# Performance work log

Measured on AMD Instinct MI355X. Metric: run time of the kernel, lower is better.

Reference implementation:

```python
import jax, jax.numpy as jnp
import numpy as np

N_EMBD = 512
N_HEAD = 8
D_HEAD = N_EMBD // N_HEAD
N_EXPERTS = 4
TOP_K = 2
D_FF = 4 * N_EMBD
EPS_RMS = 1e-5


def setup_inputs() -> dict:
    key = jax.random.key(0)
    ks = jax.random.split(key, 10)
    B, T, C = 8, 1024, N_EMBD
    s = 0.02
    return {
        "x": jax.random.normal(ks[0], (B, T, C), jnp.float32),
        "ln1_w": jnp.ones((C,), jnp.float32),
        "ln2_w": jnp.ones((C,), jnp.float32),
        "wq": jax.random.normal(ks[1], (C, C), jnp.float32) * s,
        "wk": jax.random.normal(ks[2], (C, C), jnp.float32) * s,
        "wv": jax.random.normal(ks[3], (C, C), jnp.float32) * s,
        "wo": jax.random.normal(ks[4], (C, C), jnp.float32) * s,
        "gate_w": jax.random.normal(ks[5], (N_EXPERTS, C), jnp.float32) * s,
        "w_fc": jax.random.normal(ks[6], (N_EXPERTS, D_FF, C), jnp.float32) * s,
        "w_proj": jax.random.normal(ks[7], (N_EXPERTS, C, D_FF), jnp.float32) * s,
    }


def rms_norm(x, w):
    var = jnp.mean(x * x, axis=-1, keepdims=True)
    return x * jax.lax.rsqrt(var + EPS_RMS) * w


def causal_attention(x, wq, wk, wv, wo):
    B, T, C = x.shape
    q = (x @ wq.T).reshape(B, T, N_HEAD, D_HEAD)
    k = (x @ wk.T).reshape(B, T, N_HEAD, D_HEAD)
    v = (x @ wv.T).reshape(B, T, N_HEAD, D_HEAD)
    scores = jnp.einsum("bqhd,bkhd->bhqk", q, k) / jnp.sqrt(jnp.float32(D_HEAD))
    mask = jnp.tril(jnp.ones((T, T), bool))
    scores = jnp.where(mask, scores, jnp.finfo(scores.dtype).min)
    attn = jax.nn.softmax(scores, axis=-1)
    out = jnp.einsum("bhqk,bkhd->bqhd", attn, v).reshape(B, T, C)
    return out @ wo.T


def ds_moe(x, gate_w, w_fc, w_proj):
    B, T, C = x.shape
    xf = x.reshape(B * T, C)                                # [N, C]
    gate_logits = xf @ gate_w.T                             # [N, E]
    gate_probs = jax.nn.softmax(gate_logits, axis=-1)
    topw, topi = jax.lax.top_k(gate_probs, TOP_K)           # [N, K]
    topw = topw / jnp.clip(topw.sum(-1, keepdims=True), 1e-6)
    # sparse router weights [N, E] (scatter of normalized top-k)
    sparse_w = jnp.zeros((xf.shape[0], N_EXPERTS), xf.dtype)
    sparse_w = sparse_w.at[jnp.arange(xf.shape[0])[:, None], topi].set(topw)
    # dense-equivalent expert compute: out = sum_e w_e * MLP_e(x)
    h = jax.nn.gelu(jnp.einsum("nc,efc->enf", xf, w_fc), approximate=False)
    eo = jnp.einsum("enf,ecf->enc", h, w_proj)              # [E, N, C]
    out = jnp.einsum("ne,enc->nc", sparse_w, eo)
    return out.reshape(B, T, C), sparse_w


def reference(x, ln1_w, ln2_w, wq, wk, wv, wo, gate_w, w_fc, w_proj):
    x = x + causal_attention(rms_norm(x, ln1_w), wq, wk, wv, wo)
    moe_out, router_w = ds_moe(rms_norm(x, ln2_w), gate_w, w_fc, w_proj)
    x = x + moe_out
    return x, router_w
```

## Files before the change

### kernel.cpp

```cpp
#include <hip/hip_runtime.h>
#include <math.h>

typedef __bf16 bf16_t;
typedef float    f32x2 __attribute__((ext_vector_type(2)));
typedef float    f32x4 __attribute__((ext_vector_type(4)));
typedef unsigned u32x2 __attribute__((ext_vector_type(2)));
typedef unsigned u32x4 __attribute__((ext_vector_type(4)));
typedef __bf16   bf16x8 __attribute__((ext_vector_type(8)));

#define WS_MB (size_t)(1u << 20)

__device__ __forceinline__ void gl16(const bf16_t* g, bf16_t* l) {
    void* gnc = const_cast<void*>((const void*)g);
    __builtin_amdgcn_global_load_lds((__attribute__((address_space(1))) void*)gnc,
                                     (__attribute__((address_space(3))) void*)l,
                                     16, 0, 0);
}

__device__ __forceinline__ float dot4(f32x4 a, f32x4 b) {
    return a.x * b.x + a.y * b.y + a.z * b.z + a.w * b.w;
}

__device__ __forceinline__ int xcd_swz(int orig, int nwg) {
    int q = nwg >> 3, r = nwg & 7;
    int x = orig & 7, i = orig >> 3;
    int base = (x < r) ? x * (q + 1) : r * (q + 1) + (x - r) * q;
    return base + i;
}

__global__ __launch_bounds__(256) void cvt_all_kernel(
    const float* __restrict__ s0, const float* __restrict__ s1,
    const float* __restrict__ s2, const float* __restrict__ s3,
    const float* __restrict__ s4, const float* __restrict__ s5,
    bf16_t* __restrict__ d0, bf16_t* __restrict__ d1,
    bf16_t* __restrict__ d2, bf16_t* __restrict__ d3,
    bf16_t* __restrict__ d4, bf16_t* __restrict__ d5,
    int* __restrict__ cnt) {
    if (blockIdx.x == 0 && threadIdx.x < 4) cnt[threadIdx.x] = 0;
    int i = blockIdx.x * 256 + threadIdx.x;
    const float* s; bf16_t* d; int off;
    if (i < 262144) {
        int seg = i >> 16; off = i & 65535;
        s = seg == 0 ? s0 : seg == 1 ? s1 : seg == 2 ? s2 : s3;
        d = seg == 0 ? d0 : seg == 1 ? d1 : seg == 2 ? d2 : d3;
    } else if (i < 1310720) { s = s4; d = d4; off = i - 262144; }
    else                    { s = s5; d = d5; off = i - 1310720; }
    f32x4 v = ((const f32x4*)s)[off];
    union { bf16_t b[4]; u32x2 u; } p;
    p.b[0] = (bf16_t)v.x; p.b[1] = (bf16_t)v.y;
    p.b[2] = (bf16_t)v.z; p.b[3] = (bf16_t)v.w;
    ((u32x2*)d)[off] = p.u;
}

__global__ __launch_bounds__(256) void rmsnorm_kernel(const float* __restrict__ x,
                                                      const float* __restrict__ w,
                                                      bf16_t* __restrict__ out) {
    int row = blockIdx.x;
    const float* xr = x + (size_t)row * 512;
    int t = threadIdx.x;
    f32x2 v = *(const f32x2*)(xr + t * 2);
    float ss = v.x * v.x + v.y * v.y;
#pragma unroll
    for (int o = 32; o > 0; o >>= 1) ss += __shfl_down(ss, o);
    __shared__ float red[4];
    if ((t & 63) == 0) red[t >> 6] = ss;
    __syncthreads();
    float tot = (red[0] + red[1]) + (red[2] + red[3]);
    float sc = rsqrtf(tot * (1.0f / 512.0f) + 1e-5f);
    f32x2 wv = *(const f32x2*)(w + t * 2);
    union { bf16_t b[2]; unsigned u; } p;
    p.b[0] = (bf16_t)(v.x * sc * wv.x);
    p.b[1] = (bf16_t)(v.y * sc * wv.y);
    *(unsigned*)(out + (size_t)row * 512 + t * 2) = p.u;
}

__device__ inline float gelu_fast(float x) {
    float u = -1.5957691216f * x * fmaf(0.044715f * x, x, 1.0f);
    return x / (1.0f + __expf(u));
}

#define GEMM_COMPUTE(LA, LB)                                                          \
    _Pragma("unroll")                                                                 \
    for (int kk = 0; kk < 2; ++kk) {                                                  \
        bf16x8 af[4], bfr[4];                                                         \
        _Pragma("unroll")                                                             \
        for (int mi = 0; mi < 4; mi++)                                                \
            af[mi] = *(const bf16x8*)((LA) + (wr + mi * 16 + lrow) * 64               \
                                      + (((kk * 4 + sg) ^ lr3) * 8));                 \
        _Pragma("unroll")                                                             \
        for (int ni = 0; ni < 4; ni++)                                                \
            bfr[ni] = *(const bf16x8*)((LB) + (wc + ni * 16 + lrow) * 64              \
                                       + (((kk * 4 + sg) ^ lr3) * 8));                \
        _Pragma("unroll")                                                             \
        for (int mi = 0; mi < 4; mi++) {                                              \
            _Pragma("unroll")                                                         \
            for (int ni = 0; ni < 4; ni++) {                                          \
                acc[mi][ni] = __builtin_amdgcn_mfma_f32_16x16x32_bf16(                \
                    af[mi], bfr[ni], acc[mi][ni], 0, 0, 0);                           \
            }                                                                         \
        }                                                                             \
    }

template <int EPI>
__global__ __launch_bounds__(256) void gemm_kernel(const bf16_t* __restrict__ A,
                                                   const bf16_t* __restrict__ B,
                                                   void* __restrict__ C,
                                                   const float* __restrict__ aux,
                                                   int N, int K, int ncol) {
    const int id = xcd_swz(blockIdx.x, gridDim.x);
    const int row0 = (id / ncol) * 128;
    const int col0 = (id % ncol) * 128;
    __shared__ __align__(16) bf16_t lds_a[128 * 64];
    __shared__ __align__(16) bf16_t lds_b[128 * 64];
    const int t = threadIdx.x;
    const bf16_t* Ap = A + (size_t)row0 * K;
    const bf16_t* Bp = B + (size_t)col0 * K;
    const int lane = t & 63, wave = t >> 6;
    const int wr = (wave >> 1) * 64, wc = (wave & 1) * 64;
    const int lrow = lane & 15;
    const int sg = lane >> 4, lr3 = lane & 7;
    const int srow = lane >> 3;
    const int scolx = ((lane & 7) ^ (lane >> 3)) * 8;

    f32x4 acc[4][4];
    f32x4 zero = {0.f, 0.f, 0.f, 0.f};
#pragma unroll
    for (int i = 0; i < 4; i++)
#pragma unroll
        for (int j = 0; j < 4; j++) acc[i][j] = zero;

    for (int k0 = 0; k0 < K; k0 += 64) {
        __syncthreads();
#pragma unroll
        for (int c = 0; c < 4; ++c) {
            const int rbase = wave * 32 + c * 8;
            gl16(Ap + (size_t)(rbase + srow) * K + k0 + scolx, lds_a + rbase * 64);
            gl16(Bp + (size_t)(rbase + srow) * K + k0 + scolx, lds_b + rbase * 64);
        }
        __syncthreads();
        GEMM_COMPUTE(lds_a, lds_b)
    }

#pragma unroll
    for (int mi = 0; mi < 4; mi++) {
        int rbase = row0 + wr + mi * 16 + (lane >> 4) * 4;
#pragma unroll
        for (int ni = 0; ni < 4; ni++) {
            int col = col0 + wc + ni * 16 + (lane & 15);
#pragma unroll
            for (int r = 0; r < 4; r++) {
                float v = acc[mi][ni][r];
                size_t idx = (size_t)(rbase + r) * N + col;
                if (EPI == 1) ((float*)C)[idx] = v + aux[idx];
                else          ((bf16_t*)C)[idx] = (bf16_t)v;
            }
        }
    }
}

__global__ __launch_bounds__(256) void moe_fc_kernel(
    const bf16_t* __restrict__ A, const bf16_t* __restrict__ B, bf16_t* __restrict__ H,
    const int* __restrict__ list, const int* __restrict__ cnt, const int* __restrict__ seg) {
    const int id = xcd_swz(blockIdx.x, gridDim.x);
    const int row0g = (id >> 4) * 128;
    const int col0 = (id & 15) * 128;
    int e = 0;
    if (row0g >= seg[1]) e = 1;
    if (row0g >= seg[2]) e = 2;
    if (row0g >= seg[3]) e = 3;
    const int ce = cnt[e];
    const int rl0 = row0g - seg[e];
    if (rl0 >= ce) return;

    __shared__ __align__(16) bf16_t lds_a[128 * 64];
    __shared__ __align__(16) bf16_t lds_b[128 * 64];
    const int t = threadIdx.x;
    const bf16_t* Bp = B + ((size_t)e * 2048 + col0) * 512;
    const int* le = list + e * 8192;
    const int lane = t & 63, wave = t >> 6;
    const int wr = (wave >> 1) * 64, wc = (wave & 1) * 64;
    const int lrow = lane & 15;
    const int sg = lane >> 4, lr3 = lane & 7;
    const int srow = lane >> 3;
    const int scolx = ((lane & 7) ^ (lane >> 3)) * 8;

    const bf16_t* Asrc[4];
#pragma unroll
    for (int c = 0; c < 4; ++c) {
        int r = rl0 + wave * 32 + c * 8 + srow;
        r = (r < ce) ? r : (ce - 1);
        Asrc[c] = A + (size_t)le[r] * 512 + scolx;
    }

    f32x4 acc[4][4];
    f32x4 zero = {0.f, 0.f, 0.f, 0.f};
#pragma unroll
    for (int i = 0; i < 4; i++)
#pragma unroll
        for (int j = 0; j < 4; j++) acc[i][j] = zero;

    for (int k0 = 0; k0 < 512; k0 += 64) {
        __syncthreads();
#pragma unroll
        for (int c = 0; c < 4; ++c) {
            const int rbase = wave * 32 + c * 8;
            gl16(Asrc[c] + k0, lds_a + rbase * 64);
            gl16(Bp + (size_t)(rbase + srow) * 512 + k0 + scolx, lds_b + rbase * 64);
        }
        __syncthreads();
        GEMM_COMPUTE(lds_a, lds_b)
    }

#pragma unroll
    for (int mi = 0; mi < 4; mi++) {
        int rbase = row0g + wr + mi * 16 + (lane >> 4) * 4;
#pragma unroll
        for (int ni = 0; ni < 4; ni++) {
            int col = col0 + wc + ni * 16 + (lane & 15);
#pragma unroll
            for (int r = 0; r < 4; r++) {
                H[(size_t)(rbase + r) * 2048 + col] = (bf16_t)gelu_fast(acc[mi][ni][r]);
            }
        }
    }
}

#define PJ_VMCNT0() asm volatile("s_waitcnt vmcnt(0)" ::: "memory")

#define PJ_STAGE(LA, LB, kk0)                                                          \
    _Pragma("unroll")                                                                  \
    for (int c = 0; c < 4; ++c) {                                                      \
        const int rbase = wave * 32 + c * 8;                                           \
        gl16(Ap + (size_t)(rbase + srow) * 2048 + (kk0) + scolx, (LA) + rbase * 64);   \
    }                                                                                  \
    {                                                                                  \
        const int rbase = wave * 16;                                                   \
        gl16(Bp + (size_t)(rbase + srow) * 2048 + (kk0) + scolx, (LB) + rbase * 64);   \
        gl16(Bp + (size_t)(rbase + 8 + srow) * 2048 + (kk0) + scolx,                   \
             (LB) + (rbase + 8) * 64);                                                 \
    }

#define PJ_COMPUTE(LA, LB)                                                             \
    _Pragma("unroll")                                                                  \
    for (int kk = 0; kk < 2; ++kk) {                                                   \
        bf16x8 af[4], bfr[2];                                                          \
        _Pragma("unroll")                                                              \
        for (int mi = 0; mi < 4; mi++)                                                 \
            af[mi] = *(const bf16x8*)((LA) + (wr + mi * 16 + lrow) * 64                \
                                      + (((kk * 4 + sg) ^ lr3) * 8));                  \
        _Pragma("unroll")                                                              \
        for (int ni = 0; ni < 2; ni++)                                                 \
            bfr[ni] = *(const bf16x8*)((LB) + (wc + ni * 16 + lrow) * 64               \
                                       + (((kk * 4 + sg) ^ lr3) * 8));                 \
        _Pragma("unroll")                                                              \
        for (int mi = 0; mi < 4; mi++) {                                               \
            _Pragma("unroll")                                                          \
            for (int ni = 0; ni < 2; ni++) {                                           \
                acc[mi][ni] = __builtin_amdgcn_mfma_f32_16x16x32_bf16(                 \
                    af[mi], bfr[ni], acc[mi][ni], 0, 0, 0);                            \
            }                                                                          \
        }                                                                              \
    }

__global__ __launch_bounds__(256) void moe_pj_kernel(
    const bf16_t* __restrict__ H, const bf16_t* __restrict__ B, float* __restrict__ xout,
    const float* __restrict__ rw, const int* __restrict__ list,
    const int* __restrict__ cnt, const int* __restrict__ seg) {
    const int id = xcd_swz(blockIdx.x, gridDim.x);
    const int row0g = (id >> 3) * 128;
    const int col0 = (id & 7) * 64;
    int e = 0;
    if (row0g >= seg[1]) e = 1;
    if (row0g >= seg[2]) e = 2;
    if (row0g >= seg[3]) e = 3;
    const int ce = cnt[e];
    const int se = seg[e];
    const int rl0 = row0g - se;
    if (rl0 >= ce) return;

    __shared__ __align__(16) bf16_t lds_a0[128 * 64];
    __shared__ __align__(16) bf16_t lds_a1[128 * 64];
    __shared__ __align__(16) bf16_t lds_b0[64 * 64];
    __shared__ __align__(16) bf16_t lds_b1[64 * 64];
    const int t = threadIdx.x;
    const bf16_t* Ap = H + (size_t)row0g * 2048;
    const bf16_t* Bp = B + ((size_t)e * 512 + col0) * 2048;
    const int* le = list + e * 8192;
    const int lane = t & 63, wave = t >> 6;
    const int wr = (wave >> 1) * 64, wc = (wave & 1) * 32;
    const int lrow = lane & 15;
    const int sg = lane >> 4, lr3 = lane & 7;
    const int srow = lane >> 3;
    const int scolx = ((lane & 7) ^ (lane >> 3)) * 8;

    f32x4 acc[4][2];
    f32x4 zero = {0.f, 0.f, 0.f, 0.f};
#pragma unroll
    for (int i = 0; i < 4; i++)
#pragma unroll
        for (int j = 0; j < 2; j++) acc[i][j] = zero;

    PJ_STAGE(lds_a0, lds_b0, 0)
    PJ_VMCNT0();
    __builtin_amdgcn_s_barrier();

    for (int k0 = 0; k0 < 2048; k0 += 128) {
        PJ_STAGE(lds_a1, lds_b1, k0 + 64)
        PJ_COMPUTE(lds_a0, lds_b0)
        PJ_VMCNT0();
        __builtin_amdgcn_s_barrier();
        if (k0 + 128 < 2048) { PJ_STAGE(lds_a0, lds_b0, k0 + 128) }
        PJ_COMPUTE(lds_a1, lds_b1)
        PJ_VMCNT0();
        __builtin_amdgcn_s_barrier();
    }

#pragma unroll
    for (int mi = 0; mi < 4; mi++) {
        int rbase = row0g + wr + mi * 16 + (lane >> 4) * 4;
#pragma unroll
        for (int ni = 0; ni < 2; ni++) {
            int col = col0 + wc + ni * 16 + (lane & 15);
#pragma unroll
            for (int r = 0; r < 4; r++) {
                int rloc = rbase + r - se;
                if (rloc < ce) {
                    int tok = le[rloc];
                    atomicAdd(xout + (size_t)tok * 512 + col,
                              rw[(size_t)tok * 4 + e] * acc[mi][ni][r]);
                }
            }
        }
    }
}

__global__ __launch_bounds__(256) void attn_kernel(const bf16_t* __restrict__ QKV,
                                                   bf16_t* __restrict__ O) {
    __shared__ __align__(16) bf16_t klds[2 * 64 * 32];
    __shared__ __align__(16) bf16_t vlds[4 * 2 * 16 * 32];

    const int bx = blockIdx.x;
    const int qb = 15 - (bx >> 6);
    const int bh = bx & 63;
    const int b = bh >> 3, h = bh & 7;
    const int t = threadIdx.x;
    const int lane = t & 63, wave = t >> 6;
    const int g = lane >> 4, q15 = lane & 15;
    const int qbase = qb * 64 + wave * 16;
    const int qabs = qbase + q15;

    const bf16_t* Qb = QKV + (size_t)b * 1024 * 1536 + h * 64;
    const bf16_t* Kb = Qb + 512;
    const bf16_t* Vb = Qb + 1024;

    const bf16_t* qp = Qb + (size_t)qabs * 1536 + g * 8;
    bf16x8 qf0 = *(const bf16x8*)(qp);
    bf16x8 qf1 = *(const bf16x8*)(qp + 32);

    f32x4 acc[4];
    f32x4 zero = {0.f, 0.f, 0.f, 0.f};
#pragma unroll
    for (int i = 0; i < 4; i++) acc[i] = zero;
    float m = -1e30f, denom = 0.f;

    const int kr1 = t >> 3, kc1 = t & 7;
    const int vr = t & 63, vc1 = t >> 6, vc2 = vc1 + 4;
    const int perm = ((q15 >> 2) * 8) + (q15 & 3);

    const int nkt = qb + 1;
    for (int kt = 0; kt < nkt; ++kt) {
        u32x4 ka  = *(const u32x4*)(Kb + (size_t)(kt * 64 + kr1) * 1536 + kc1 * 8);
        u32x4 kb2 = *(const u32x4*)(Kb + (size_t)(kt * 64 + kr1 + 32) * 1536 + kc1 * 8);
        u32x4 va  = *(const u32x4*)(Vb + (size_t)(kt * 64 + vr) * 1536 + vc1 * 8);
        u32x4 vb2 = *(const u32x4*)(Vb + (size_t)(kt * 64 + vr) * 1536 + vc2 * 8);
        __syncthreads();
        *(u32x4*)(klds + (kc1 >> 2) * 2048 + kr1 * 32 + (kc1 & 3) * 8) = ka;
        *(u32x4*)(klds + (kc1 >> 2) * 2048 + (kr1 + 32) * 32 + (kc1 & 3) * 8) = kb2;
        {
            union { u32x4 u; bf16_t e[8]; } tv;
            const int kh = vr >> 5, k32 = vr & 31;
            tv.u = va;
#pragma unroll
            for (int j = 0; j < 8; ++j) {
                int d = vc1 * 8 + j;
                vlds[(((d >> 4) * 2 + kh) * 16 + (d & 15)) * 32 + k32] = tv.e[j];
            }
            tv.u = vb2;
#pragma unroll
            for (int j = 0; j < 8; ++j) {
                int d = vc2 * 8 + j;
                vlds[(((d >> 4) * 2 + kh) * 16 + (d & 15)) * 32 + k32] = tv.e[j];
            }
        }
        __syncthreads();

        for (int s32 = 0; s32 < 2; ++s32) {
            const int KB = kt * 64 + s32 * 32;
            if (KB > qbase + 15) break;
            const int r0 = s32 * 32 + perm;
            bf16x8 k00 = *(const bf16x8*)(klds + r0 * 32 + g * 8);
            bf16x8 k01 = *(const bf16x8*)(klds + 2048 + r0 * 32 + g * 8);
            bf16x8 k10 = *(const bf16x8*)(klds + (r0 + 4) * 32 + g * 8);
            bf16x8 k11 = *(const bf16x8*)(klds + 2048 + (r0 + 4) * 32 + g * 8);
            f32x4 s0 = zero, s1 = zero;
            s0 = __builtin_amdgcn_mfma_f32_16x16x32_bf16(k00, qf0, s0, 0, 0, 0);
            s0 = __builtin_amdgcn_mfma_f32_16x16x32_bf16(k01, qf1, s0, 0, 0, 0);
            s1 = __builtin_amdgcn_mfma_f32_16x16x32_bf16(k10, qf0, s1, 0, 0, 0);
            s1 = __builtin_amdgcn_mfma_f32_16x16x32_bf16(k11, qf1, s1, 0, 0, 0);

            const int kbg = KB + 8 * g;
            float sv[8];
#pragma unroll
            for (int r = 0; r < 4; ++r) {
                sv[r]     = (kbg + r     <= qabs) ? s0[r] * 0.125f : -1e30f;
                sv[4 + r] = (kbg + 4 + r <= qabs) ? s1[r] * 0.125f : -1e30f;
            }
            float tm = sv[0];
#pragma unroll
            for (int j = 1; j < 8; ++j) tm = fmaxf(tm, sv[j]);
            tm = fmaxf(tm, __shfl_xor(tm, 16));
            tm = fmaxf(tm, __shfl_xor(tm, 32));
            const float mn = fmaxf(m, tm);
            const float co = __expf(m - mn);
            float p[8];
            float ts = 0.f;
#pragma unroll
            for (int j = 0; j < 8; ++j) { p[j] = __expf(sv[j] - mn); ts += p[j]; }
            ts += __shfl_xor(ts, 16);
            ts += __shfl_xor(ts, 32);
            denom = denom * co + ts;
            m = mn;
            union { bf16_t e[8]; bf16x8 v; } pp;
#pragma unroll
            for (int j = 0; j < 8; ++j) pp.e[j] = (bf16_t)p[j];

#pragma unroll
            for (int db = 0; db < 4; ++db) {
                acc[db] *= co;
                bf16x8 vf = *(const bf16x8*)(vlds + ((db * 2 + s32) * 16 + q15) * 32 + g * 8);
                acc[db] = __builtin_amdgcn_mfma_f32_16x16x32_bf16(vf, pp.v, acc[db], 0, 0, 0);
            }
        }
    }

    const float inv = 1.0f / denom;
    bf16_t* op = O + (size_t)b * 1024 * 512 + h * 64 + (size_t)qabs * 512;
#pragma unroll
    for (int db = 0; db < 4; ++db) {
        union { bf16_t e[4]; u32x2 u; } w;
#pragma unroll
        for (int r = 0; r < 4; ++r) w.e[r] = (bf16_t)(acc[db][r] * inv);
        *(u32x2*)(op + db * 16 + g * 4) = w.u;
    }
}

__global__ void seg_kernel(const int* __restrict__ cnt, int* __restrict__ seg) {
    if (threadIdx.x == 0) {
        int b = 0;
#pragma unroll
        for (int e = 0; e < 4; ++e) { seg[e] = b; b += (cnt[e] + 127) & ~127; }
    }
}

__global__ __launch_bounds__(256) void router_kernel(
    const float* __restrict__ xr, const float* __restrict__ w,
    const float* __restrict__ gw, bf16_t* __restrict__ hb,
    float* __restrict__ rout, int* __restrict__ list, int* __restrict__ cnt) {
    __shared__ int lcnt[4], gb[4];
    __shared__ int ent_tok[64], ent_e[64], ent_r[64];
    const int t = threadIdx.x, lane = t & 63, wave = t >> 6;
    if (t < 4) lcnt[t] = 0;
    __syncthreads();

    const f32x4 w0  = *(const f32x4*)(w + lane * 8);
    const f32x4 w1  = *(const f32x4*)(w + lane * 8 + 4);
    const f32x4 g00 = *(const f32x4*)(gw + lane * 8);
    const f32x4 g01 = *(const f32x4*)(gw + lane * 8 + 4);
    const f32x4 g10 = *(const f32x4*)(gw + 512 + lane * 8);
    const f32x4 g11 = *(const f32x4*)(gw + 512 + lane * 8 + 4);
    const f32x4 g20 = *(const f32x4*)(gw + 1024 + lane * 8);
    const f32x4 g21 = *(const f32x4*)(gw + 1024 + lane * 8 + 4);
    const f32x4 g30 = *(const f32x4*)(gw + 1536 + lane * 8);
    const f32x4 g31 = *(const f32x4*)(gw + 1536 + lane * 8 + 4);

    for (int it = 0; it < 8; ++it) {
        const int tok = blockIdx.x * 32 + wave * 8 + it;
        const float* row = xr + (size_t)tok * 512 + lane * 8;
        f32x4 v0 = *(const f32x4*)(row);
        f32x4 v1 = *(const f32x4*)(row + 4);
        float ss = dot4(v0, v0) + dot4(v1, v1);
        f32x4 xw0, xw1;
        xw0.x = v0.x * w0.x; xw0.y = v0.y * w0.y; xw0.z = v0.z * w0.z; xw0.w = v0.w * w0.w;
        xw1.x = v1.x * w1.x; xw1.y = v1.y * w1.y; xw1.z = v1.z * w1.z; xw1.w = v1.w * w1.w;
        float d0 = dot4(xw0, g00) + dot4(xw1, g01);
        float d1 = dot4(xw0, g10) + dot4(xw1, g11);
        float d2 = dot4(xw0, g20) + dot4(xw1, g21);
        float d3 = dot4(xw0, g30) + dot4(xw1, g31);
#pragma unroll
        for (int o = 32; o > 0; o >>= 1) {
            ss += __shfl_xor(ss, o);
            d0 += __shfl_xor(d0, o);
            d1 += __shfl_xor(d1, o);
            d2 += __shfl_xor(d2, o);
            d3 += __shfl_xor(d3, o);
        }
        const float sc = rsqrtf(ss * (1.0f / 512.0f) + 1e-5f);
        union { bf16_t b[8]; u32x4 u; } hw;
        hw.b[0] = (bf16_t)(xw0.x * sc); hw.b[1] = (bf16_t)(xw0.y * sc);
        hw.b[2] = (bf16_t)(xw0.z * sc); hw.b[3] = (bf16_t)(xw0.w * sc);
        hw.b[4] = (bf16_t)(xw1.x * sc); hw.b[5] = (bf16_t)(xw1.y * sc);
        hw.b[6] = (bf16_t)(xw1.z * sc); hw.b[7] = (bf16_t)(xw1.w * sc);
        *(u32x4*)(hb + (size_t)tok * 512 + lane * 8) = hw.u;

        const float l0 = d0 * sc, l1 = d1 * sc, l2 = d2 * sc, l3 = d3 * sc;
        float mx = fmaxf(fmaxf(l0, l1), fmaxf(l2, l3));
        float p[4];
        p[0] = expf(l0 - mx); p[1] = expf(l1 - mx);
        p[2] = expf(l2 - mx); p[3] = expf(l3 - mx);
        float s = (p[0] + p[1]) + (p[2] + p[3]);
        float is = 1.0f / s;
        p[0] *= is; p[1] *= is; p[2] *= is; p[3] *= is;
        int i0 = 0; float b0 = p[0];
#pragma unroll
        for (int e = 1; e < 4; e++) if (p[e] > b0) { b0 = p[e]; i0 = e; }
        int i1 = -1; float b1 = -1.f;
#pragma unroll
        for (int e = 0; e < 4; e++) {
            if (e == i0) continue;
            if (p[e] > b1) { b1 = p[e]; i1 = e; }
        }
        if (lane == 0) {
            float inv2 = 1.0f / fmaxf(b0 + b1, 1e-6f);
            float o[4] = {0.f, 0.f, 0.f, 0.f};
            o[i0] = b0 * inv2;
            o[i1] = b1 * inv2;
            f32x4 ov; ov.x = o[0]; ov.y = o[1]; ov.z = o[2]; ov.w = o[3];
            *(f32x4*)(rout + (size_t)tok * 4) = ov;
            int r0 = atomicAdd(&lcnt[i0], 1);
            int r1 = atomicAdd(&lcnt[i1], 1);
            int ei = (wave * 8 + it) * 2;
            ent_tok[ei] = tok;     ent_e[ei] = i0;     ent_r[ei] = r0;
            ent_tok[ei + 1] = tok; ent_e[ei + 1] = i1; ent_r[ei + 1] = r1;
        }
    }
    __syncthreads();
    if (t < 4) gb[t] = atomicAdd(&cnt[t], lcnt[t]);
    __syncthreads();
    if (t < 64) {
        int e = ent_e[t];
        list[e * 8192 + gb[e] + ent_r[t]] = ent_tok[t];
    }
}

extern "C" void kernel_launch(void* const* d_in, const int* in_sizes, int n_in,
                              void* d_out, int out_size, void* d_ws, size_t ws_size,
                              hipStream_t stream) {
    (void)in_sizes; (void)n_in; (void)out_size; (void)ws_size;
    const float* x   = (const float*)d_in[0];
    const float* ln1 = (const float*)d_in[1];
    const float* ln2 = (const float*)d_in[2];
    const float* wq  = (const float*)d_in[3];
    const float* wk  = (const float*)d_in[4];
    const float* wv  = (const float*)d_in[5];
    const float* wo  = (const float*)d_in[6];
    const float* gw  = (const float*)d_in[7];
    const float* wfc = (const float*)d_in[8];
    const float* wpj = (const float*)d_in[9];

    char* ws = (char*)d_ws;
    bf16_t* hb    = (bf16_t*)(ws);
    bf16_t* qkvb  = (bf16_t*)(ws + 8 * WS_MB);
    bf16_t* attb  = (bf16_t*)(ws + 32 * WS_MB);
    bf16_t* Hb    = (bf16_t*)(ws + 8 * WS_MB);
    bf16_t* wqkvb = (bf16_t*)(ws + 74 * WS_MB);
    bf16_t* wob   = (bf16_t*)(ws + 74 * WS_MB + 1536 * 1024);
    bf16_t* wfcb  = (bf16_t*)(ws + 76 * WS_MB);
    bf16_t* wpjb  = (bf16_t*)(ws + 84 * WS_MB);
    int*    list  = (int*)(ws + 92 * WS_MB);
    int*    cnt   = (int*)(ws + 92 * WS_MB + 192 * 1024);
    int*    seg   = cnt + 8;

    float* xout   = (float*)d_out;
    float* router = xout + (size_t)8192 * 512;

    cvt_all_kernel<<<9216, 256, 0, stream>>>(wq, wk, wv, wo, wfc, wpj,
                                             wqkvb, wqkvb + 512 * 512, wqkvb + 1024 * 512,
                                             wob, wfcb, wpjb, cnt);

    rmsnorm_kernel<<<8192, 256, 0, stream>>>(x, ln1, hb);
    gemm_kernel<4><<<768, 256, 0, stream>>>(hb, wqkvb, (void*)qkvb, nullptr, 1536, 512, 12);

    attn_kernel<<<1024, 256, 0, stream>>>(qkvb, attb);

    gemm_kernel<1><<<256, 256, 0, stream>>>(attb, wob, (void*)xout, x, 512, 512, 4);

    router_kernel<<<256, 256, 0, stream>>>(xout, ln2, gw, hb, router, list, cnt);
    seg_kernel<<<1, 64, 0, stream>>>(cnt, seg);

    moe_fc_kernel<<<16 * 131, 256, 0, stream>>>(hb, wfcb, Hb, list, cnt, seg);
    moe_pj_kernel<<<8 * 131, 256, 0, stream>>>(Hb, wpjb, xout, router, list, cnt, seg);
}
```

Baseline: 265.6 us.

## Triple-buffer MoE projection loads and prefetch next K/V tile in attention

The MoE down-projection GEMM moves from a double-buffered LDS scheme with full vmcnt(0) waits to a three-stage ring buffer. Each iteration waits only for the older stage (vmcnt(6)) and uses a single barrier per 64-wide k step. The attention kernel register-prefetches the next K/V tile after the LDS writes, so global load latency overlaps the current tile's compute. This costs 50% more LDS in the projection kernel, which may lower occupancy, and extra registers for the prefetched tiles.

```diff
diff --git a/kernel.cpp b/kernel.cpp
--- a/kernel.cpp
+++ b/kernel.cpp
@@ -225,8 +225,6 @@
     }
 }
 
-#define PJ_VMCNT0() asm volatile("s_waitcnt vmcnt(0)" ::: "memory")
-
 #define PJ_STAGE(LA, LB, kk0)                                                          \
     _Pragma("unroll")                                                                  \
     for (int c = 0; c < 4; ++c) {                                                      \
@@ -278,10 +276,8 @@
     const int rl0 = row0g - se;
     if (rl0 >= ce) return;
 
-    __shared__ __align__(16) bf16_t lds_a0[128 * 64];
-    __shared__ __align__(16) bf16_t lds_a1[128 * 64];
-    __shared__ __align__(16) bf16_t lds_b0[64 * 64];
-    __shared__ __align__(16) bf16_t lds_b1[64 * 64];
+    __shared__ __align__(16) bf16_t a0[128 * 64], a1[128 * 64], a2[128 * 64];
+    __shared__ __align__(16) bf16_t b0[64 * 64],  b1[64 * 64],  b2[64 * 64];
     const int t = threadIdx.x;
     const bf16_t* Ap = H + (size_t)row0g * 2048;
     const bf16_t* Bp = B + ((size_t)e * 512 + col0) * 2048;
@@ -300,20 +296,23 @@
 #pragma unroll
         for (int j = 0; j < 2; j++) acc[i][j] = zero;
 
-    PJ_STAGE(lds_a0, lds_b0, 0)
-    PJ_VMCNT0();
+    PJ_STAGE(a0, b0, 0)
+    PJ_STAGE(a1, b1, 64)
+    bf16_t *cA = a0, *cB = b0, *nA = a1, *nB = b1, *fA = a2, *fB = b2;
+
+    for (int k0 = 0; k0 < 1984; k0 += 64) {
+        asm volatile("s_waitcnt vmcnt(6)" ::: "memory");
+        __builtin_amdgcn_sched_barrier(0);
+        __builtin_amdgcn_s_barrier();
+        if (k0 + 128 < 2048) { PJ_STAGE(fA, fB, k0 + 128) }
+        PJ_COMPUTE(cA, cB)
+        bf16_t* t1 = cA; cA = nA; nA = fA; fA = t1;
+        bf16_t* t2 = cB; cB = nB; nB = fB; fB = t2;
+    }
+    asm volatile("s_waitcnt vmcnt(0)" ::: "memory");
+    __builtin_amdgcn_sched_barrier(0);
     __builtin_amdgcn_s_barrier();
-
-    for (int k0 = 0; k0 < 2048; k0 += 128) {
-        PJ_STAGE(lds_a1, lds_b1, k0 + 64)
-        PJ_COMPUTE(lds_a0, lds_b0)
-        PJ_VMCNT0();
-        __builtin_amdgcn_s_barrier();
-        if (k0 + 128 < 2048) { PJ_STAGE(lds_a0, lds_b0, k0 + 128) }
-        PJ_COMPUTE(lds_a1, lds_b1)
-        PJ_VMCNT0();
-        __builtin_amdgcn_s_barrier();
-    }
+    PJ_COMPUTE(cA, cB)
 
 #pragma unroll
     for (int mi = 0; mi < 4; mi++) {
@@ -368,11 +367,12 @@
     const int perm = ((q15 >> 2) * 8) + (q15 & 3);
 
     const int nkt = qb + 1;
+    u32x4 ka  = *(const u32x4*)(Kb + (size_t)(kr1) * 1536 + kc1 * 8);
+    u32x4 kb2 = *(const u32x4*)(Kb + (size_t)(kr1 + 32) * 1536 + kc1 * 8);
+    u32x4 va  = *(const u32x4*)(Vb + (size_t)(vr) * 1536 + vc1 * 8);
+    u32x4 vb2 = *(const u32x4*)(Vb + (size_t)(vr) * 1536 + vc2 * 8);
+
     for (int kt = 0; kt < nkt; ++kt) {
-        u32x4 ka  = *(const u32x4*)(Kb + (size_t)(kt * 64 + kr1) * 1536 + kc1 * 8);
-        u32x4 kb2 = *(const u32x4*)(Kb + (size_t)(kt * 64 + kr1 + 32) * 1536 + kc1 * 8);
-        u32x4 va  = *(const u32x4*)(Vb + (size_t)(kt * 64 + vr) * 1536 + vc1 * 8);
-        u32x4 vb2 = *(const u32x4*)(Vb + (size_t)(kt * 64 + vr) * 1536 + vc2 * 8);
         __syncthreads();
         *(u32x4*)(klds + (kc1 >> 2) * 2048 + kr1 * 32 + (kc1 & 3) * 8) = ka;
         *(u32x4*)(klds + (kc1 >> 2) * 2048 + (kr1 + 32) * 32 + (kc1 & 3) * 8) = kb2;
@@ -393,6 +393,14 @@
             }
         }
         __syncthreads();
+
+        if (kt + 1 < nkt) {
+            const size_t krow = (size_t)((kt + 1) * 64);
+            ka  = *(const u32x4*)(Kb + (krow + kr1) * 1536 + kc1 * 8);
+            kb2 = *(const u32x4*)(Kb + (krow + kr1 + 32) * 1536 + kc1 * 8);
+            va  = *(const u32x4*)(Vb + (krow + vr) * 1536 + vc1 * 8);
+            vb2 = *(const u32x4*)(Vb + (krow + vr) * 1536 + vc2 * 8);
+        }
 
         for (int s32 = 0; s32 < 2; ++s32) {
             const int KB = kt * 64 + s32 * 32;
```

Result: slower. 299.6 us (+12.8%).
